# Kernel optimization log

Measured on AMD Instinct MI355X. Metric: run time of the kernel, lower is better.

## Reference

```python
import jax, jax.numpy as jnp
import numpy as np

N_RAYS = 8192
N_SURF = 2048
EPS = 1e-18  # matches torch zero-denominator patch value


def setup_inputs() -> dict:
    key = jax.random.key(0)
    k1, k2, k3 = jax.random.split(key, 3)
    o = jax.random.normal(k1, (N_RAYS, 3), dtype=jnp.float32)
    d = jax.random.normal(k2, (N_RAYS, 3), dtype=jnp.float32)
    V = jax.random.normal(k3, (N_SURF, 4, 3), dtype=jnp.float32)
    return {"o": o, "d": d, "V": V}


def _safe(x):
    # torch code sets exact-zero denominators to 1e-18 via nonzero() indexing
    return jnp.where(x == 0.0, EPS, x)


def reference(o, d, V):
    # --- get_intersections: ray-plane intersection scalars t (N, M) ---
    v = jnp.cross(V[:, 1] - V[:, 0], V[:, 2] - V[:, 0])          # (M,3) plane normals
    v = v / jnp.linalg.norm(v, axis=1, keepdims=True)
    k = -jnp.sum(v * V[:, 3], axis=1)                             # (M,) plane offsets
    vo = o @ v.T                                                  # (N,M)
    vd = d @ v.T                                                  # (N,M)
    t = -(k[None, :] + vo) / vd                                   # (N,M)

    # intersection points r = o + t*d, broadcast over surfaces -> (N,M,3)
    r = o[:, None, :] + t[..., None] * d[:, None, :]

    # --- get_onsurface_surface_intersections: barycentric masking ---
    a = V[None, :, 0]  # (1,M,3) broadcast instead of .repeat
    b = V[None, :, 1]
    c = V[None, :, 2]
    ax, ay, az = a[..., 0], a[..., 1], a[..., 2]
    rx, ry, rz = r[..., 0], r[..., 1], r[..., 2]

    A = ax * rz - az * rx
    B = ax * b[..., 2] - az * b[..., 0]
    C = ax * ry - ay * rx
    D = ax * b[..., 1] - ay * b[..., 0]
    E = ax * c[..., 2] - az * c[..., 0]
    F = B * (ay * c[..., 0] - ax * c[..., 1])
    G = D

    gam = (G * (A * D - B * C)) / _safe(D * (E * G + F))          # (N,M)
    beta = (C + gam * (ay * c[..., 0] - ax * c[..., 1])) / _safe(D)
    alpha = (rx - (beta * b[..., 0] + gam * c[..., 0])) / _safe(ax)

    mask = (beta > 0.0) & (gam > 0.0) & (alpha > 0.0)             # (N,M) bool
    return t * mask.astype(t.dtype)                               # masked intersection depths
```

## Files before the change

kernel.cpp:

```cpp
#include <hip/hip_runtime.h>


#define N_RAYS 8192
#define N_SURF 2048
constexpr int RPB = 32;

__device__ __forceinline__ float safef(float x) {
    return (x == 0.0f) ? 1e-18f : x;
}

__global__ __launch_bounds__(256, 8) void trace_kernel(
    const float* __restrict__ o, const float* __restrict__ dr,
    const float* __restrict__ V, float* __restrict__ out)
{
    const int s = blockIdx.x * 256 + threadIdx.x;

    const float4 p0 = *(const float4*)(V + (size_t)s * 12);
    const float4 p1 = *(const float4*)(V + (size_t)s * 12 + 4);
    const float4 p2 = *(const float4*)(V + (size_t)s * 12 + 8);
    const float ax = p0.x, ay = p0.y, az = p0.z;
    const float bx = p0.w, by = p1.x, bz = p1.y;
    const float cx = p1.z, cy = p1.w, cz = p2.x;
    const float wx = p2.y, wy = p2.z, wz = p2.w;

    const float e0x = bx - ax, e0y = by - ay, e0z = bz - az;
    const float e1x = cx - ax, e1y = cy - ay, e1z = cz - az;
    const float nx = e0y * e1z - e0z * e1y;
    const float ny = e0z * e1x - e0x * e1z;
    const float nz = e0x * e1y - e0y * e1x;
    const float rn = __builtin_amdgcn_rsqf(fmaf(nx, nx, fmaf(ny, ny, nz * nz)));
    const float vx = nx * rn, vy = ny * rn, vz = nz * rn;
    const float k = -fmaf(vx, wx, fmaf(vy, wy, vz * wz));

    const float B  = ax * bz - az * bx;
    const float D  = ax * by - ay * bx;
    const float E  = ax * cz - az * cx;
    const float P  = ay * cx - ax * cy;
    const float F  = B * P;
    const float rden = __builtin_amdgcn_rcpf(safef(D * fmaf(E, D, F)));
    const float rD   = __builtin_amdgcn_rcpf(safef(D));
    const float rAX  = __builtin_amdgcn_rcpf(safef(ax));

    const float DB = D * B, DD = D * D;
    const float g0 = (DB * ay - DD * az) * rden;
    const float g1 = -(DB * ax) * rden;
    const float g2 = (DD * ax) * rden;
    const float bp  = P * rD;
    const float bb0 = fmaf(bp, g0, -ay * rD);
    const float bb1 = fmaf(bp, g1,  ax * rD);
    const float bb2 = bp * g2;
    const float ab = -bx * rAX, ac = -cx * rAX;
    const float aa0 = fmaf(ab, bb0, fmaf(ac, g0, rAX));
    const float aa1 = fmaf(ab, bb1, ac * g1);
    const float aa2 = fmaf(ab, bb2, ac * g2);

    const int ray0 = blockIdx.y * RPB;
    float* outp = out + (size_t)ray0 * N_SURF + s;
#pragma unroll 4
    for (int i = 0; i < RPB; ++i) {
        const int ray = ray0 + i;
        const float o0 = o[ray * 3 + 0], o1 = o[ray * 3 + 1], o2 = o[ray * 3 + 2];
        const float d0 = dr[ray * 3 + 0], d1 = dr[ray * 3 + 1], d2 = dr[ray * 3 + 2];

        const float vo_k = fmaf(o0, vx, fmaf(o1, vy, fmaf(o2, vz, k)));
        const float vd   = fmaf(d0, vx, fmaf(d1, vy, d2 * vz));
        const float t    = -vo_k * __builtin_amdgcn_rcpf(vd);

        const float rx = fmaf(t, d0, o0);
        const float ry = fmaf(t, d1, o1);
        const float rz = fmaf(t, d2, o2);

        const float gam   = fmaf(g0,  rx, fmaf(g1,  ry, g2  * rz));
        const float beta  = fmaf(bb0, rx, fmaf(bb1, ry, bb2 * rz));
        const float alpha = fmaf(aa0, rx, fmaf(aa1, ry, aa2 * rz));

        const float mn = fminf(fminf(beta, gam), alpha);
        outp[(size_t)i * N_SURF] = (mn > 0.0f) ? t : 0.0f;
    }
}

extern "C" void kernel_launch(void* const* d_in, const int* in_sizes, int n_in,
                              void* d_out, int out_size, void* d_ws, size_t ws_size,
                              hipStream_t stream) {
    const float* o  = (const float*)d_in[0];
    const float* dr = (const float*)d_in[1];
    const float* V  = (const float*)d_in[2];
    float* out = (float*)d_out;

    trace_kernel<<<dim3(N_SURF / 256, N_RAYS / RPB), dim3(256), 0, stream>>>(o, dr, V, out);
}
```

Measured before the change: 84.92 us.

## Precompute per-surface coefficients in separate kernel and use packed float2 math

```diff
diff --git a/kernel.cpp b/kernel.cpp
--- a/kernel.cpp
+++ b/kernel.cpp
@@ -3,15 +3,18 @@
 
 #define N_RAYS 8192
 #define N_SURF 2048
-constexpr int RPB = 32;
+constexpr int RPB = 16;
+constexpr int SPT = 2;
+
+typedef float v2f __attribute__((ext_vector_type(2)));
+#define FMA2(a, b, c) __builtin_elementwise_fma((a), (b), (c))
 
 __device__ __forceinline__ float safef(float x) {
     return (x == 0.0f) ? 1e-18f : x;
 }
 
-__global__ __launch_bounds__(256, 8) void trace_kernel(
-    const float* __restrict__ o, const float* __restrict__ dr,
-    const float* __restrict__ V, float* __restrict__ out)
+__global__ __launch_bounds__(256) void coeff_kernel(
+    const float* __restrict__ V, float* __restrict__ cf)
 {
     const int s = blockIdx.x * 256 + threadIdx.x;
 
@@ -54,28 +57,73 @@
     const float aa1 = fmaf(ab, bb1, ac * g1);
     const float aa2 = fmaf(ab, bb2, ac * g2);
 
+    cf[ 0 * N_SURF + s] = vx;
+    cf[ 1 * N_SURF + s] = vy;
+    cf[ 2 * N_SURF + s] = vz;
+    cf[ 3 * N_SURF + s] = k;
+    cf[ 4 * N_SURF + s] = g0;
+    cf[ 5 * N_SURF + s] = g1;
+    cf[ 6 * N_SURF + s] = g2;
+    cf[ 7 * N_SURF + s] = bb0;
+    cf[ 8 * N_SURF + s] = bb1;
+    cf[ 9 * N_SURF + s] = bb2;
+    cf[10 * N_SURF + s] = aa0;
+    cf[11 * N_SURF + s] = aa1;
+    cf[12 * N_SURF + s] = aa2;
+}
+
+__global__ __launch_bounds__(256, 8) void trace_kernel(
+    const float* __restrict__ o, const float* __restrict__ dr,
+    const float* __restrict__ cf, float* __restrict__ out)
+{
+    const int s0 = (blockIdx.x * 256 + threadIdx.x) * SPT;
+
+    const v2f vx  = *(const v2f*)(cf +  0 * N_SURF + s0);
+    const v2f vy  = *(const v2f*)(cf +  1 * N_SURF + s0);
+    const v2f vz  = *(const v2f*)(cf +  2 * N_SURF + s0);
+    const v2f kk  = *(const v2f*)(cf +  3 * N_SURF + s0);
+    const v2f g0  = *(const v2f*)(cf +  4 * N_SURF + s0);
+    const v2f g1  = *(const v2f*)(cf +  5 * N_SURF + s0);
+    const v2f g2  = *(const v2f*)(cf +  6 * N_SURF + s0);
+    const v2f bb0 = *(const v2f*)(cf +  7 * N_SURF + s0);
+    const v2f bb1 = *(const v2f*)(cf +  8 * N_SURF + s0);
+    const v2f bb2 = *(const v2f*)(cf +  9 * N_SURF + s0);
+    const v2f aa0 = *(const v2f*)(cf + 10 * N_SURF + s0);
+    const v2f aa1 = *(const v2f*)(cf + 11 * N_SURF + s0);
+    const v2f aa2 = *(const v2f*)(cf + 12 * N_SURF + s0);
+
     const int ray0 = blockIdx.y * RPB;
-    float* outp = out + (size_t)ray0 * N_SURF + s;
+    float* outp = out + (size_t)ray0 * N_SURF + s0;
+
 #pragma unroll 4
     for (int i = 0; i < RPB; ++i) {
         const int ray = ray0 + i;
         const float o0 = o[ray * 3 + 0], o1 = o[ray * 3 + 1], o2 = o[ray * 3 + 2];
         const float d0 = dr[ray * 3 + 0], d1 = dr[ray * 3 + 1], d2 = dr[ray * 3 + 2];
+        const v2f o0v = o0, o1v = o1, o2v = o2;
+        const v2f d0v = d0, d1v = d1, d2v = d2;
 
-        const float vo_k = fmaf(o0, vx, fmaf(o1, vy, fmaf(o2, vz, k)));
-        const float vd   = fmaf(d0, vx, fmaf(d1, vy, d2 * vz));
-        const float t    = -vo_k * __builtin_amdgcn_rcpf(vd);
+        const v2f vo_k = FMA2(o0v, vx, FMA2(o1v, vy, FMA2(o2v, vz, kk)));
+        const v2f vd   = FMA2(d0v, vx, FMA2(d1v, vy, d2v * vz));
+        v2f rv;
+        rv.x = __builtin_amdgcn_rcpf(vd.x);
+        rv.y = __builtin_amdgcn_rcpf(vd.y);
+        const v2f t = -vo_k * rv;
 
-        const float rx = fmaf(t, d0, o0);
-        const float ry = fmaf(t, d1, o1);
-        const float rz = fmaf(t, d2, o2);
+        const v2f rx = FMA2(t, d0v, o0v);
+        const v2f ry = FMA2(t, d1v, o1v);
+        const v2f rz = FMA2(t, d2v, o2v);
 
-        const float gam   = fmaf(g0,  rx, fmaf(g1,  ry, g2  * rz));
-        const float beta  = fmaf(bb0, rx, fmaf(bb1, ry, bb2 * rz));
-        const float alpha = fmaf(aa0, rx, fmaf(aa1, ry, aa2 * rz));
+        const v2f gam = FMA2(g0,  rx, FMA2(g1,  ry, g2  * rz));
+        const v2f bet = FMA2(bb0, rx, FMA2(bb1, ry, bb2 * rz));
+        const v2f alp = FMA2(aa0, rx, FMA2(aa1, ry, aa2 * rz));
 
-        const float mn = fminf(fminf(beta, gam), alpha);
-        outp[(size_t)i * N_SURF] = (mn > 0.0f) ? t : 0.0f;
+        const float mnx = fminf(fminf(bet.x, gam.x), alp.x);
+        const float mny = fminf(fminf(bet.y, gam.y), alp.y);
+        v2f res;
+        res.x = (mnx > 0.0f) ? t.x : 0.0f;
+        res.y = (mny > 0.0f) ? t.y : 0.0f;
+        *(v2f*)(outp + (size_t)i * N_SURF) = res;
     }
 }
 
@@ -86,6 +134,8 @@
     const float* dr = (const float*)d_in[1];
     const float* V  = (const float*)d_in[2];
     float* out = (float*)d_out;
+    float* cf  = (float*)d_ws;
 
-    trace_kernel<<<dim3(N_SURF / 256, N_RAYS / RPB), dim3(256), 0, stream>>>(o, dr, V, out);
+    coeff_kernel<<<dim3(N_SURF / 256), dim3(256), 0, stream>>>(V, cf);
+    trace_kernel<<<dim3(N_SURF / (256 * SPT), N_RAYS / RPB), dim3(256), 0, stream>>>(o, dr, cf, out);
 }
```

After: 86.20 us. Within noise of the previous version (+1.5%).
